# Kernel tuning notes

Measured on AMD Instinct MI355X. Metric: run time of the kernel, lower is better.

The kernel has to match this reference:

```python
import jax, jax.numpy as jnp
import numpy as np

ANCHOR_SIZES = (128.0, 256.0, 512.0)
ASPECT_RATIOS = (0.5, 1.0, 2.0)
NMS_THR = 0.7
KEEP_PRE = 1000    # test_keep_pre_nms
KEEP_POST = 300    # test_keep_post_nms


def make_anchors(fh, fw, img_h, img_w):
    # base anchors per (ratio, size), centered at origin, xyxy
    sizes = jnp.array(ANCHOR_SIZES, jnp.float32)
    ratios = jnp.array(ASPECT_RATIOS, jnp.float32)
    h_r = jnp.sqrt(ratios)
    w_r = 1.0 / h_r
    ws = (w_r[:, None] * sizes[None, :]).reshape(-1)  # [nA]
    hs = (h_r[:, None] * sizes[None, :]).reshape(-1)
    base = jnp.stack([-ws, -hs, ws, hs], axis=1) / 2.0  # [nA,4]
    stride_h = img_h / fh
    stride_w = img_w / fw
    sx = jnp.arange(fw, dtype=jnp.float32) * stride_w
    sy = jnp.arange(fh, dtype=jnp.float32) * stride_h
    yy, xx = jnp.meshgrid(sy, sx, indexing='ij')
    shifts = jnp.stack([xx, yy, xx, yy], axis=-1).reshape(-1, 1, 4)  # [fh*fw,1,4]
    return (shifts + base[None]).reshape(-1, 4)  # [fh*fw*nA,4]


def offsets2boxes(deltas, anchors):
    # deltas: [bs,N,4] (dx,dy,dw,dh); anchors: [N,4] xyxy
    aw = anchors[:, 2] - anchors[:, 0]
    ah = anchors[:, 3] - anchors[:, 1]
    acx = anchors[:, 0] + 0.5 * aw
    acy = anchors[:, 1] + 0.5 * ah
    pcx = deltas[..., 0] * aw + acx
    pcy = deltas[..., 1] * ah + acy
    pw = jnp.exp(deltas[..., 2]) * aw
    ph = jnp.exp(deltas[..., 3]) * ah
    return jnp.stack([pcx - 0.5 * pw, pcy - 0.5 * ph,
                      pcx + 0.5 * pw, pcy + 0.5 * ph], axis=-1)


def nms_single(boxes, scores):
    # boxes [K,4] already sorted by descending score; sequential greedy NMS
    K = boxes.shape[0]
    b = jax.lax.stop_gradient(boxes)
    area = (b[:, 2] - b[:, 0]) * (b[:, 3] - b[:, 1])
    lt = jnp.maximum(b[:, None, :2], b[None, :, :2])
    rb = jnp.minimum(b[:, None, 2:], b[None, :, 2:])
    wh = jnp.clip(rb - lt, 0.0)
    inter = wh[..., 0] * wh[..., 1]
    iou = inter / (area[:, None] + area[None, :] - inter + 1e-9)  # [K,K]
    idx = jnp.arange(K)

    def body(i, keep):
        suppress = (iou[i] > NMS_THR) & keep[i] & (idx > i)
        return keep & ~suppress

    keep = jax.lax.fori_loop(0, K, body, jnp.ones((K,), bool))
    # stable: kept boxes first, preserving score order; pad to KEEP_POST
    order = jnp.argsort((~keep).astype(jnp.int32))[:KEEP_POST]
    valid = keep[order].astype(boxes.dtype)
    dets = jnp.concatenate([boxes[order], scores[order, None]], axis=-1)
    return dets * valid[:, None]  # padded rows are zeros


def setup_inputs() -> dict:
    key = jax.random.key(0)
    ks = jax.random.split(key, 4)
    C = 512
    nA = 9
    return {
        'fmaps': jax.random.normal(ks[0], (8, C, 64, 64), jnp.float32),
        'base_w': jax.random.normal(ks[1], (C, C, 3, 3), jnp.float32) * 0.01,
        'base_b': jnp.zeros((C,), jnp.float32),
        'cls_w': jax.random.normal(ks[2], (nA, C), jnp.float32) * 0.01,
        'cls_b': jnp.zeros((nA,), jnp.float32),
        'reg_w': jax.random.normal(ks[3], (nA * 4, C), jnp.float32) * 0.01,
        'reg_b': jnp.zeros((nA * 4,), jnp.float32),
        'img_h': 1024,
        'img_w': 1024,
    }


def reference(fmaps, base_w, base_b, cls_w, cls_b, reg_w, reg_b, img_h, img_w):
    bs, C, fh, fw = fmaps.shape
    nA = len(ANCHOR_SIZES) * len(ASPECT_RATIOS)
    # PredictionLayer: 3x3 conv + relu, then 1x1 cls / reg convs
    x = jax.lax.conv_general_dilated(
        fmaps, base_w, window_strides=(1, 1), padding='SAME',
        dimension_numbers=('NCHW', 'OIHW', 'NCHW'))
    x = jax.nn.relu(x + base_b[None, :, None, None])
    cls = jnp.einsum('bchw,ac->bahw', x, cls_w) + cls_b[None, :, None, None]
    reg = jnp.einsum('bchw,ac->bahw', x, reg_w) + reg_b[None, :, None, None]
    # flatten_preds: view(bs,nA,c,h,w) -> permute(0,3,4,1,2) -> (bs, h*w*nA, c)
    cls_logits = cls.reshape(bs, nA, 1, fh, fw).transpose(0, 3, 4, 1, 2).reshape(bs, -1, 1)
    reg_deltas = reg.reshape(bs, nA, 4, fh, fw).transpose(0, 3, 4, 1, 2).reshape(bs, -1, 4)
    # DetectionLayer
    anchors = make_anchors(fh, fw, float(img_h), float(img_w))
    scores = jax.nn.sigmoid(cls_logits[..., 0])          # [bs, N]
    boxes = offsets2boxes(reg_deltas, anchors)           # [bs, N, 4]
    _, sel = jax.lax.top_k(scores, KEEP_PRE)             # per-image top-k
    s = jnp.take_along_axis(scores, sel, axis=1)
    b = jnp.take_along_axis(boxes, sel[..., None], axis=1)
    # clip boxes to image
    b = jnp.stack([jnp.clip(b[..., 0], 0.0, float(img_w)),
                   jnp.clip(b[..., 1], 0.0, float(img_h)),
                   jnp.clip(b[..., 2], 0.0, float(img_w)),
                   jnp.clip(b[..., 3], 0.0, float(img_h))], axis=-1)
    # per-image NMS; output padded to fixed [bs, KEEP_POST, 5]
    return jax.vmap(nms_single)(b, s)
```

## Files before the change

### kernel.cpp

```cpp
#include <hip/hip_runtime.h>
#include <math.h>


typedef double f64x4 __attribute__((ext_vector_type(4)));
typedef double f64x2 __attribute__((ext_vector_type(2)));

#define BS 8
#define CIN 512
#define COUT 512
#define FH 64
#define FW 64
#define NA 9
#define NPIX (FH*FW)
#define NANCH (NPIX*NA)
#define NPAD 65536
#define KPRE 1000
#define KPOST 300

#define OFF_X      0ull
#define OFF_SCORES (OFF_X + 134217728ull)
#define OFF_BOXES  (OFF_SCORES + 2359296ull)
#define OFF_KEYS   (OFF_BOXES + 9437184ull)
#define OFF_BUF1   (OFF_KEYS + 4194304ull)
#define OFF_BUF2   (OFF_BUF1 + 1048576ull)
#define OFF_SEL    (OFF_BUF2 + 262144ull)
#define OFF_KEEP   (OFF_SEL + 32768ull)
#define WS_NEEDED  (OFF_KEEP + 32768ull)
#define OFF_MASK   OFF_X
#define WOFF_U        WS_NEEDED
#define WOFF_V        (WOFF_U + 33554432ull)
#define WS_WINO_FULL  (WOFF_V + 67108864ull + 67108864ull)
#define WS_WINO_HALF  (WOFF_V + 33554432ull + 33554432ull)

#define SW_STRIDE 80
#define SW_WORDS  (36 * SW_STRIDE)
#define SI_RSTRIDE 80
#define SI_CSTRIDE 320
#define BUF_WORDS (SW_WORDS + 4 * SI_CSTRIDE)

__device__ __forceinline__ void conv_compute(
    const float* __restrict__ sWp, const float* __restrict__ sIp,
    const int* __restrict__ boff, f64x4 acc[2][4]) {
#pragma unroll
  for (int k0s = 0; k0s < 9; ++k0s) {
    double a0 = (double)sWp[k0s * 4 * SW_STRIDE];
    double a1 = (double)sWp[k0s * 4 * SW_STRIDE + 16];
    const float* bp = sIp + boff[k0s];
    double b0 = (double)bp[0];
    double b1 = (double)bp[16];
    double b2 = (double)bp[32];
    double b3 = (double)bp[48];
    acc[0][0] = __builtin_amdgcn_mfma_f64_16x16x4f64(a0, b0, acc[0][0], 0, 0, 0);
    acc[0][1] = __builtin_amdgcn_mfma_f64_16x16x4f64(a0, b1, acc[0][1], 0, 0, 0);
    acc[0][2] = __builtin_amdgcn_mfma_f64_16x16x4f64(a0, b2, acc[0][2], 0, 0, 0);
    acc[0][3] = __builtin_amdgcn_mfma_f64_16x16x4f64(a0, b3, acc[0][3], 0, 0, 0);
    acc[1][0] = __builtin_amdgcn_mfma_f64_16x16x4f64(a1, b0, acc[1][0], 0, 0, 0);
    acc[1][1] = __builtin_amdgcn_mfma_f64_16x16x4f64(a1, b1, acc[1][1], 0, 0, 0);
    acc[1][2] = __builtin_amdgcn_mfma_f64_16x16x4f64(a1, b2, acc[1][2], 0, 0, 0);
    acc[1][3] = __builtin_amdgcn_mfma_f64_16x16x4f64(a1, b3, acc[1][3], 0, 0, 0);
  }
}

__global__ __launch_bounds__(256, 3) void conv_mfma_kernel(
    const float* __restrict__ fm, const float* __restrict__ W,
    const float* __restrict__ bias, double* __restrict__ x) {
  __shared__ float sbuf[2 * BUF_WORDS];
  const int ocb = blockIdx.x, rp = blockIdx.y, b = blockIdx.z;
  const int h0 = rp * 2;
  const int oc0 = ocb * 64;
  const int tid = threadIdx.x;
  const int wid = tid >> 6, l = tid & 63;
  const int q = l >> 4, r16 = l & 15;
  const int wm = wid >> 1, wn = wid & 1;

  const int wo = tid >> 2, wseg = tid & 3;
  const float* wbase = W + (size_t)(oc0 + wo) * 4608 + wseg * 9;
  const int wlds0 = (wseg * 9) * SW_STRIDE + wo;

  const float* fmb = fm + (size_t)b * CIN * NPIX;
  int ioff[5];
  int idls[5];
  bool sact[5], lact[5];
#pragma unroll
  for (int s = 0; s < 5; ++s) {
    int li = tid + 256 * s;
    sact[s] = li < 1056;
    int li_c = sact[s] ? li : 0;
    int c = li_c / 264, rem = li_c % 264, r = rem / 66, col = rem % 66;
    int gy = h0 - 1 + r, gx = col - 1;
    lact[s] = sact[s] && gy >= 0 && gy < FH && gx >= 0 && gx < FW;
    ioff[s] = lact[s] ? (c * NPIX + gy * FW + gx) : 0;
    idls[s] = SW_WORDS + c * SI_CSTRIDE + r * SI_RSTRIDE + col;
  }

  const int apos = q * SW_STRIDE + wm * 32 + r16;
  const int ipos = SW_WORDS + wn * SI_RSTRIDE + r16;
  int boff[9];
#pragma unroll
  for (int k0s = 0; k0s < 9; ++k0s) {
    int k = k0s * 4 + q;
    int c = k / 9, t = k - 9 * c;
    int dy = t / 3, dx = t - 3 * dy;
    boff[k0s] = c * SI_CSTRIDE + dy * SI_RSTRIDE + dx;
  }

  f64x4 acc[2][4];
#pragma unroll
  for (int tm = 0; tm < 2; ++tm)
#pragma unroll
    for (int tn = 0; tn < 4; ++tn)
#pragma unroll
      for (int v = 0; v < 4; ++v) acc[tm][tn][v] = 0.0;

  float wreg[9], ireg[5];

#define LOAD_REGS(t) do {                                            \
    const int cc_ = 4 * (t);                                         \
    _Pragma("unroll")                                                \
    for (int j = 0; j < 9; ++j) wreg[j] = wbase[cc_ * 9 + j];        \
    _Pragma("unroll")                                                \
    for (int s = 0; s < 5; ++s)                                      \
      ireg[s] = lact[s] ? fmb[(size_t)(ioff[s] + cc_ * NPIX)] : 0.f; \
  } while (0)

#define WRITE_LDS(base) do {                                         \
    _Pragma("unroll")                                                \
    for (int j = 0; j < 9; ++j) (base)[wlds0 + j * SW_STRIDE] = wreg[j]; \
    _Pragma("unroll")                                                \
    for (int s = 0; s < 5; ++s)                                      \
      if (sact[s]) (base)[idls[s]] = ireg[s];                        \
  } while (0)

  float* buf0 = sbuf;
  float* buf1 = sbuf + BUF_WORDS;

  LOAD_REGS(0);
  WRITE_LDS(buf0);
  __syncthreads();

  for (int tt = 0; tt < 64; ++tt) {
    const int t1 = 2 * tt + 1;
    LOAD_REGS(t1);
    __builtin_amdgcn_s_setprio(1);
    conv_compute(buf0 + apos, buf0 + ipos, boff, acc);
    __builtin_amdgcn_s_setprio(0);
    WRITE_LDS(buf1);
    __syncthreads();
    const int t2 = (t1 + 1 < 128) ? t1 + 1 : 127;
    LOAD_REGS(t2);
    __builtin_amdgcn_s_setprio(1);
    conv_compute(buf1 + apos, buf1 + ipos, boff, acc);
    __builtin_amdgcn_s_setprio(0);
    WRITE_LDS(buf0);
    __syncthreads();
  }

  int prow[4], pcol[4];
  {
    f64x4 probe = {0.0, 0.0, 0.0, 0.0};
    double pa = (q == 0) ? (double)r16 : ((q == 1) ? 1.0 : 0.0);
    double pb = (q == 0) ? 1.0 : ((q == 1) ? (double)(16 * r16) : 0.0);
    probe = __builtin_amdgcn_mfma_f64_16x16x4f64(pa, pb, probe, 0, 0, 0);
#pragma unroll
    for (int v = 0; v < 4; ++v) {
      int val = (int)(probe[v] + 0.5);
      prow[v] = val & 15;
      pcol[v] = (val >> 4) & 15;
    }
  }

#pragma unroll
  for (int tm = 0; tm < 2; ++tm) {
#pragma unroll
    for (int v = 0; v < 4; ++v) {
      const int oc = oc0 + wm * 32 + tm * 16 + prow[v];
      const double bv = (double)bias[oc];
      const int h = h0 + wn;
#pragma unroll
      for (int tn = 0; tn < 4; ++tn) {
        const int w = tn * 16 + pcol[v];
        double val = acc[tm][tn][v] + bv;
        val = val > 0.0 ? val : 0.0;
        x[(size_t)(b * COUT + oc) * NPIX + h * FW + w] = val;
      }
    }
  }
#undef LOAD_REGS
#undef WRITE_LDS
}

__global__ __launch_bounds__(256) void wino_wt_kernel(
    const float* __restrict__ W, double* __restrict__ U) {
  const int id = blockIdx.x * 256 + threadIdx.x;
  const int oc = id >> 9, c = id & 511;
  const float* g = W + (size_t)(oc * CIN + c) * 9;
  double g0[3], g1[3], g2[3];
#pragma unroll
  for (int j = 0; j < 3; ++j) {
    g0[j] = (double)g[j];
    g1[j] = (double)g[3 + j];
    g2[j] = (double)g[6 + j];
  }
  double T[4][3];
#pragma unroll
  for (int j = 0; j < 3; ++j) {
    T[0][j] = g0[j];
    T[1][j] = 0.5 * (g0[j] + g1[j] + g2[j]);
    T[2][j] = 0.5 * (g0[j] - g1[j] + g2[j]);
    T[3][j] = g2[j];
  }
  double* Ub = U + (size_t)c * 512 + oc;
#pragma unroll
  for (int xi = 0; xi < 4; ++xi) {
    double u0 = T[xi][0];
    double u1 = 0.5 * (T[xi][0] + T[xi][1] + T[xi][2]);
    double u2 = 0.5 * (T[xi][0] - T[xi][1] + T[xi][2]);
    double u3 = T[xi][2];
    Ub[(size_t)(xi * 4 + 0) * 262144] = u0;
    Ub[(size_t)(xi * 4 + 1) * 262144] = u1;
    Ub[(size_t)(xi * 4 + 2) * 262144] = u2;
    Ub[(size_t)(xi * 4 + 3) * 262144] = u3;
  }
}

template <int T>
__global__ __launch_bounds__(256) void wino_in_kernel(
    const float* __restrict__ fm, double* __restrict__ V, int b, int t0) {
  const int id = blockIdx.x * 256 + threadIdx.x;
  const int c = id / T, rem = id % T;
  const int tyx = t0 + rem;
  const int ty = tyx >> 5, tx = tyx & 31;
  const float* src = fm + (size_t)(b * CIN + c) * NPIX;
  const int y0 = 2 * ty - 1, x0 = 2 * tx - 1;
  double d[4][4];
#pragma unroll
  for (int r = 0; r < 4; ++r) {
    int y = y0 + r;
#pragma unroll
    for (int s = 0; s < 4; ++s) {
      int xx = x0 + s;
      d[r][s] = (y >= 0 && y < FH && xx >= 0 && xx < FW)
                    ? (double)src[y * FW + xx] : 0.0;
    }
  }
  double Z[4][4];
#pragma unroll
  for (int s = 0; s < 4; ++s) {
    Z[0][s] = d[0][s] - d[2][s];
    Z[1][s] = d[1][s] + d[2][s];
    Z[2][s] = d[2][s] - d[1][s];
    Z[3][s] = d[1][s] - d[3][s];
  }
  double* Vb = V + (size_t)c * T + rem;
#pragma unroll
  for (int xi = 0; xi < 4; ++xi) {
    double v0 = Z[xi][0] - Z[xi][2];
    double v1 = Z[xi][1] + Z[xi][2];
    double v2 = Z[xi][2] - Z[xi][1];
    double v3 = Z[xi][1] - Z[xi][3];
    Vb[(size_t)(xi * 4 + 0) * 512 * T] = v0;
    Vb[(size_t)(xi * 4 + 1) * 512 * T] = v1;
    Vb[(size_t)(xi * 4 + 2) * 512 * T] = v2;
    Vb[(size_t)(xi * 4 + 3) * 512 * T] = v3;
  }
}

#define WSU_STRIDE 72
#define WSV_STRIDE 136
#define WSU_WORDS  (8 * WSU_STRIDE)
#define WBUF_WORDS (WSU_WORDS + 8 * WSV_STRIDE)

__device__ __forceinline__ void wino_compute(
    const double* __restrict__ sA, const double* __restrict__ sB,
    f64x4 acc[2][4]) {
#pragma unroll
  for (int kg = 0; kg < 2; ++kg) {
    double a0 = sA[kg * 4 * WSU_STRIDE];
    double a1 = sA[kg * 4 * WSU_STRIDE + 16];
    const double* bp = sB + kg * 4 * WSV_STRIDE;
    double b0 = bp[0];
    double b1 = bp[16];
    double b2 = bp[32];
    double b3 = bp[48];
    acc[0][0] = __builtin_amdgcn_mfma_f64_16x16x4f64(a0, b0, acc[0][0], 0, 0, 0);
    acc[0][1] = __builtin_amdgcn_mfma_f64_16x16x4f64(a0, b1, acc[0][1], 0, 0, 0);
    acc[0][2] = __builtin_amdgcn_mfma_f64_16x16x4f64(a0, b2, acc[0][2], 0, 0, 0);
    acc[0][3] = __builtin_amdgcn_mfma_f64_16x16x4f64(a0, b3, acc[0][3], 0, 0, 0);
    acc[1][0] = __builtin_amdgcn_mfma_f64_16x16x4f64(a1, b0, acc[1][0], 0, 0, 0);
    acc[1][1] = __builtin_amdgcn_mfma_f64_16x16x4f64(a1, b1, acc[1][1], 0, 0, 0);
    acc[1][2] = __builtin_amdgcn_mfma_f64_16x16x4f64(a1, b2, acc[1][2], 0, 0, 0);
    acc[1][3] = __builtin_amdgcn_mfma_f64_16x16x4f64(a1, b3, acc[1][3], 0, 0, 0);
  }
}

template <int T>
__global__ __launch_bounds__(256, 3) void wino_gemm_kernel(
    const double* __restrict__ U, const double* __restrict__ V,
    double* __restrict__ M) {
  __shared__ double sbuf[2 * WBUF_WORDS];
  const int ocb = blockIdx.x, tb = blockIdx.y, pos = blockIdx.z;
  const int oc0 = ocb * 64, t0 = tb * 128;
  const int tid = threadIdx.x;
  const int wid = tid >> 6, l = tid & 63;
  const int q = l >> 4, r16 = l & 15;
  const int wm = wid >> 1, wn = wid & 1;

  const int ka = tid >> 5;
  const int oc2 = (tid & 31) * 2;
  const int t4 = (tid & 31) * 4;
  const double* uSrc = U + (size_t)pos * 262144 + (size_t)ka * 512 + oc0 + oc2;
  const double* vSrc = V + (size_t)pos * 512 * T + (size_t)ka * T + t0 + t4;
  const int ua_lds = ka * WSU_STRIDE + oc2;
  const int vb_lds = WSU_WORDS + ka * WSV_STRIDE + t4;

  const int apos = q * WSU_STRIDE + wm * 32 + r16;
  const int bpos = WSU_WORDS + q * WSV_STRIDE + wn * 64 + r16;

  f64x4 acc[2][4];
#pragma unroll
  for (int tm = 0; tm < 2; ++tm)
#pragma unroll
    for (int tn = 0; tn < 4; ++tn)
#pragma unroll
      for (int v = 0; v < 4; ++v) acc[tm][tn][v] = 0.0;

  f64x2 ra, rb0, rb1;

#define WLOAD(t) do {                                                  \
    const size_t cc_ = 8 * (size_t)(t);                                \
    ra  = *(const f64x2*)(uSrc + cc_ * 512);                           \
    rb0 = *(const f64x2*)(vSrc + cc_ * T);                             \
    rb1 = *(const f64x2*)(vSrc + cc_ * T + 2);                         \
  } while (0)

#define WSTORE(base) do {                                              \
    (base)[ua_lds] = ra[0]; (base)[ua_lds + 1] = ra[1];                \
    (base)[vb_lds] = rb0[0]; (base)[vb_lds + 1] = rb0[1];              \
    (base)[vb_lds + 2] = rb1[0]; (base)[vb_lds + 3] = rb1[1];          \
  } while (0)

  double* buf0 = sbuf;
  double* buf1 = sbuf + WBUF_WORDS;

  WLOAD(0);
  WSTORE(buf0);
  __syncthreads();

  for (int tt = 0; tt < 32; ++tt) {
    const int t1 = 2 * tt + 1;
    WLOAD(t1);
    __builtin_amdgcn_s_setprio(1);
    wino_compute(buf0 + apos, buf0 + bpos, acc);
    __builtin_amdgcn_s_setprio(0);
    WSTORE(buf1);
    __syncthreads();
    const int t2 = (t1 + 1 < 64) ? t1 + 1 : 63;
    WLOAD(t2);
    __builtin_amdgcn_s_setprio(1);
    wino_compute(buf1 + apos, buf1 + bpos, acc);
    __builtin_amdgcn_s_setprio(0);
    WSTORE(buf0);
    __syncthreads();
  }

  int prow[4], pcol[4];
  {
    f64x4 probe = {0.0, 0.0, 0.0, 0.0};
    double pa = (q == 0) ? (double)r16 : ((q == 1) ? 1.0 : 0.0);
    double pb = (q == 0) ? 1.0 : ((q == 1) ? (double)(16 * r16) : 0.0);
    probe = __builtin_amdgcn_mfma_f64_16x16x4f64(pa, pb, probe, 0, 0, 0);
#pragma unroll
    for (int v = 0; v < 4; ++v) {
      int val = (int)(probe[v] + 0.5);
      prow[v] = val & 15;
      pcol[v] = (val >> 4) & 15;
    }
  }

#pragma unroll
  for (int tm = 0; tm < 2; ++tm) {
#pragma unroll
    for (int v = 0; v < 4; ++v) {
      const int oc = oc0 + wm * 32 + tm * 16 + prow[v];
#pragma unroll
      for (int tn = 0; tn < 4; ++tn) {
        const int col = wn * 64 + tn * 16 + pcol[v];
        M[(size_t)pos * 512 * T + (size_t)oc * T + t0 + col] = acc[tm][tn][v];
      }
    }
  }
#undef WLOAD
#undef WSTORE
}

template <int T>
__global__ __launch_bounds__(256) void wino_out_kernel(
    const double* __restrict__ M, const float* __restrict__ bias,
    double* __restrict__ x, int b, int t0) {
  const int id = blockIdx.x * 256 + threadIdx.x;
  const int oc = id / T, rem = id % T;
  const int tyx = t0 + rem;
  const int ty = tyx >> 5, tx = tyx & 31;
  double m[4][4];
#pragma unroll
  for (int xi = 0; xi < 4; ++xi)
#pragma unroll
    for (int nu = 0; nu < 4; ++nu)
      m[xi][nu] = M[(size_t)(xi * 4 + nu) * 512 * T + (size_t)oc * T + rem];
  double P[2][4];
#pragma unroll
  for (int nu = 0; nu < 4; ++nu) {
    P[0][nu] = m[0][nu] + m[1][nu] + m[2][nu];
    P[1][nu] = m[1][nu] - m[2][nu] - m[3][nu];
  }
  const double bv = (double)bias[oc];
  double* xb = x + (size_t)(b * COUT + oc) * NPIX + (2 * ty) * FW + 2 * tx;
#pragma unroll
  for (int i = 0; i < 2; ++i) {
    double y0 = P[i][0] + P[i][1] + P[i][2] + bv;
    double y1 = P[i][1] - P[i][2] - P[i][3] + bv;
    y0 = y0 > 0.0 ? y0 : 0.0;
    y1 = y1 > 0.0 ? y1 : 0.0;
    xb[i * FW] = y0;
    xb[i * FW + 1] = y1;
  }
}

#define HX_STRIDE 72
#define HW_STRIDE 52
#define HSX_WORDS (16 * HX_STRIDE)
#define HBUF_WORDS (HSX_WORDS + 16 * HW_STRIDE)

__device__ __forceinline__ void heads_compute(
    const double* __restrict__ sA, const double* __restrict__ sB,
    f64x4 acc[3]) {
#pragma unroll
  for (int k0s = 0; k0s < 4; ++k0s) {
    double a0 = sA[k0s * 4 * HW_STRIDE];
    double a1 = sA[k0s * 4 * HW_STRIDE + 16];
    double a2 = sA[k0s * 4 * HW_STRIDE + 32];
    double b0 = sB[k0s * 4 * HX_STRIDE];
    acc[0] = __builtin_amdgcn_mfma_f64_16x16x4f64(a0, b0, acc[0], 0, 0, 0);
    acc[1] = __builtin_amdgcn_mfma_f64_16x16x4f64(a1, b0, acc[1], 0, 0, 0);
    acc[2] = __builtin_amdgcn_mfma_f64_16x16x4f64(a2, b0, acc[2], 0, 0, 0);
  }
}

__global__ __launch_bounds__(256) void heads_mfma_kernel(
    const double* __restrict__ x, const float* __restrict__ cls_w,
    const float* __restrict__ cls_b, const float* __restrict__ reg_w,
    const float* __restrict__ reg_b, const int* __restrict__ img_h,
    const int* __restrict__ img_w, double* __restrict__ scores,
    double* __restrict__ boxes, unsigned long long* __restrict__ keys) {
  __shared__ double sh[2 * HBUF_WORDS];
  const int pxb = blockIdx.x, b = blockIdx.y;
  const int tid = threadIdx.x;
  const int wid = tid >> 6, l = tid & 63;
  const int q = l >> 4, r16 = l & 15;
  const int wn = wid;

  const double* xbase = x + (size_t)b * CIN * NPIX + pxb * 64;
  int sxk[4], sxp[4];
#pragma unroll
  for (int s = 0; s < 4; ++s) {
    int i = tid + 256 * s;
    sxk[s] = i >> 6; sxp[s] = i & 63;
  }
  int swk[3], swo[3];
#pragma unroll
  for (int s = 0; s < 3; ++s) {
    int i = tid + 256 * s;
    swk[s] = i / 48; swo[s] = i % 48;
  }

  const int aposh = HSX_WORDS + q * HW_STRIDE + r16;
  const int bposh = q * HX_STRIDE + wn * 16 + r16;

  f64x4 acc[3];
#pragma unroll
  for (int mt = 0; mt < 3; ++mt)
#pragma unroll
    for (int v = 0; v < 4; ++v) acc[mt][v] = 0.0;

  double xr[4], wr[3];

#define HLOAD(t) do {                                                    \
    const int cc_ = 16 * (t);                                            \
    _Pragma("unroll")                                                    \
    for (int s = 0; s < 4; ++s)                                          \
      xr[s] = xbase[(size_t)(cc_ + sxk[s]) * NPIX + sxp[s]];             \
    _Pragma("unroll")                                                    \
    for (int s = 0; s < 3; ++s) {                                        \
      int o = swo[s], k = cc_ + swk[s];                                  \
      wr[s] = (o < 9) ? (double)cls_w[o * CIN + k]                       \
            : (o < 45) ? (double)reg_w[(o - 9) * CIN + k] : 0.0;         \
    }                                                                    \
  } while (0)

#define HSTORE(base) do {                                                \
    _Pragma("unroll")                                                    \
    for (int s = 0; s < 4; ++s) (base)[sxk[s] * HX_STRIDE + sxp[s]] = xr[s]; \
    _Pragma("unroll")                                                    \
    for (int s = 0; s < 3; ++s)                                          \
      (base)[HSX_WORDS + swk[s] * HW_STRIDE + swo[s]] = wr[s];           \
  } while (0)

  double* buf0 = sh;
  double* buf1 = sh + HBUF_WORDS;

  HLOAD(0);
  HSTORE(buf0);
  __syncthreads();

  for (int tt = 0; tt < 16; ++tt) {
    const int t1 = 2 * tt + 1;
    HLOAD(t1);
    __builtin_amdgcn_s_setprio(1);
    heads_compute(buf0 + aposh, buf0 + bposh, acc);
    __builtin_amdgcn_s_setprio(0);
    HSTORE(buf1);
    __syncthreads();
    const int t2 = (t1 + 1 < 32) ? t1 + 1 : 31;
    HLOAD(t2);
    __builtin_amdgcn_s_setprio(1);
    heads_compute(buf1 + aposh, buf1 + bposh, acc);
    __builtin_amdgcn_s_setprio(0);
    HSTORE(buf0);
    __syncthreads();
  }

  int prow[4], pcol[4];
  {
    f64x4 probe = {0.0, 0.0, 0.0, 0.0};
    double pa = (q == 0) ? (double)r16 : ((q == 1) ? 1.0 : 0.0);
    double pb = (q == 0) ? 1.0 : ((q == 1) ? (double)(16 * r16) : 0.0);
    probe = __builtin_amdgcn_mfma_f64_16x16x4f64(pa, pb, probe, 0, 0, 0);
#pragma unroll
    for (int v = 0; v < 4; ++v) {
      int val = (int)(probe[v] + 0.5);
      prow[v] = val & 15;
      pcol[v] = (val >> 4) & 15;
    }
  }

  double* slog = sh;
#pragma unroll
  for (int mt = 0; mt < 3; ++mt) {
#pragma unroll
    for (int v = 0; v < 4; ++v) {
      const int o = mt * 16 + prow[v];
      if (o < 45) {
        double bv = (o < 9) ? (double)cls_b[o] : (double)reg_b[o - 9];
        slog[o * HX_STRIDE + wn * 16 + pcol[v]] = acc[mt][v] + bv;
      }
    }
  }
  __syncthreads();

  const double ih = (double)img_h[0], iw = (double)img_w[0];
  const double sth = ih / (double)FH, stw = iw / (double)FW;
  const double ratios[3] = {0.5, 1.0, 2.0};
  const double sizes[3] = {128.0, 256.0, 512.0};

  for (int it = tid; it < 576; it += 256) {
    int px = it / 9, a = it % 9;
    int p = pxb * 64 + px;
    int hh = p >> 6, ww = p & 63;
    double z = slog[a * HX_STRIDE + px];
    double score = 1.0 / (1.0 + exp(-z));
    double d0 = slog[(9 + a * 4 + 0) * HX_STRIDE + px];
    double d1 = slog[(9 + a * 4 + 1) * HX_STRIDE + px];
    double d2 = slog[(9 + a * 4 + 2) * HX_STRIDE + px];
    double d3 = slog[(9 + a * 4 + 3) * HX_STRIDE + px];
    double ratio = ratios[a / 3], size = sizes[a % 3];
    double hr = sqrt(ratio), wr_ = 1.0 / hr;
    double wsz = wr_ * size, hsz = hr * size;
    double sxc = (double)ww * stw, syc = (double)hh * sth;
    double ax0 = sxc - wsz * 0.5, ax1 = sxc + wsz * 0.5;
    double ay0 = syc - hsz * 0.5, ay1 = syc + hsz * 0.5;
    double aw = ax1 - ax0, ah = ay1 - ay0;
    double acx = ax0 + 0.5 * aw, acy = ay0 + 0.5 * ah;
    double pcx = d0 * aw + acx, pcy = d1 * ah + acy;
    double pw = exp(d2) * aw, ph = exp(d3) * ah;
    double bx0 = pcx - 0.5 * pw, by0 = pcy - 0.5 * ph;
    double bx1 = pcx + 0.5 * pw, by1 = pcy + 0.5 * ph;
    bx0 = fmin(fmax(bx0, 0.0), iw); bx1 = fmin(fmax(bx1, 0.0), iw);
    by0 = fmin(fmax(by0, 0.0), ih); by1 = fmin(fmax(by1, 0.0), ih);
    long n = (long)p * 9 + a;
    long base = (long)b * NANCH + n;
    boxes[base * 4 + 0] = bx0; boxes[base * 4 + 1] = by0;
    boxes[base * 4 + 2] = bx1; boxes[base * 4 + 3] = by1;
    scores[base] = score;
    unsigned long long bits = (unsigned long long)__double_as_longlong(score);
    keys[(long)b * NPAD + n] =
        ~((bits & 0xFFFFFFFFFFFF0000ull) | (0xFFFFull - (unsigned long long)n));
  }
#undef HLOAD
#undef HSTORE
}

__device__ inline void bitonic4096(unsigned long long* s, int tid) {
  for (int k = 2; k <= 4096; k <<= 1) {
    for (int j = k >> 1; j > 0; j >>= 1) {
#pragma unroll 2
      for (int t = tid; t < 2048; t += 1024) {
        int i = ((t & ~(j - 1)) << 1) | (t & (j - 1));
        int p = i | j;
        bool up = ((i & k) == 0);
        unsigned long long a = s[i], c = s[p];
        if ((a > c) == up) { s[i] = c; s[p] = a; }
      }
      __syncthreads();
    }
  }
}

__global__ __launch_bounds__(1024) void sort_topk_kernel(
    const unsigned long long* __restrict__ in, unsigned long long* __restrict__ out,
    long in_stride, long out_stride) {
  __shared__ unsigned long long s[4096];
  const int b = blockIdx.y, q = blockIdx.x, tid = threadIdx.x;
  const unsigned long long* ip = in + (long)b * in_stride + (long)q * 4096;
#pragma unroll 4
  for (int l = tid; l < 4096; l += 1024) s[l] = ip[l];
  __syncthreads();
  bitonic4096(s, tid);
  unsigned long long* op = out + (long)b * out_stride + (long)q * 1024;
  op[tid] = s[tid];
}

__global__ __launch_bounds__(1024) void sort_final_kernel(
    const unsigned long long* __restrict__ in, int* __restrict__ sel) {
  __shared__ unsigned long long s[4096];
  const int b = blockIdx.x, tid = threadIdx.x;
  const unsigned long long* ip = in + (long)b * 4096;
#pragma unroll 4
  for (int l = tid; l < 4096; l += 1024) s[l] = ip[l];
  __syncthreads();
  bitonic4096(s, tid);
  if (tid < KPRE) sel[b * 1024 + tid] = (int)(s[tid] & 0xFFFFull);
}

__global__ __launch_bounds__(256) void nms_mask_kernel(
    const double* __restrict__ boxes, const int* __restrict__ sel,
    unsigned long long* __restrict__ mask) {
  __shared__ double X0[KPRE], Y0[KPRE], X1[KPRE], Y1[KPRE], AR[KPRE];
  const int ig = blockIdx.x, b = blockIdx.y, tid = threadIdx.x;
  for (int r = tid; r < KPRE; r += 256) {
    int n = sel[b * 1024 + r];
    const double* bp = boxes + ((long)b * NANCH + n) * 4;
    double x0 = bp[0], y0 = bp[1], x1 = bp[2], y1 = bp[3];
    X0[r] = x0; Y0[r] = y0; X1[r] = x1; Y1[r] = y1;
    AR[r] = (x1 - x0) * (y1 - y0);
  }
  __syncthreads();
  const int i = ig * 16 + (tid >> 4);
  const int w = tid & 15;
  if (i >= KPRE) return;
  const double xi0 = X0[i], yi0 = Y0[i], xi1 = X1[i], yi1 = Y1[i], ai = AR[i];
  unsigned long long m = 0;
#pragma unroll 8
  for (int jj = 0; jj < 64; ++jj) {
    int jo = (jj + w) & 63;
    int j = w * 64 + jo;
    if (j < KPRE && j > i) {
      double lx = fmax(xi0, X0[j]), ly = fmax(yi0, Y0[j]);
      double rx = fmin(xi1, X1[j]), ry = fmin(yi1, Y1[j]);
      double ww_ = fmax(rx - lx, 0.0);
      double hh_ = fmax(ry - ly, 0.0);
      double inter = ww_ * hh_;
      double iou = inter / (ai + AR[j] - inter + 1e-9);
      if (iou > 0.7) m |= (1ull << jo);
    }
  }
  mask[((size_t)b * 1024 + i) * 16 + w] = m;
}

__global__ __launch_bounds__(256) void nms_scan_kernel(
    const unsigned long long* __restrict__ mask, int* __restrict__ keep) {
  __shared__ unsigned long long smask[16384];
  __shared__ unsigned long long skeep[16];
  const int b = blockIdx.x, tid = threadIdx.x;
  const unsigned long long* mb = mask + (size_t)b * 1024 * 16;
  for (int l = tid; l < KPRE * 16; l += 256) smask[l] = mb[l];
  __syncthreads();
  if (tid < 64) {
    const int lane16 = tid & 15;
    unsigned long long mykeep = ~0ull;
    unsigned long long p0, p1, p2, p3, p4, p5, p6, p7,
                       p8, p9, p10, p11, p12, p13, p14, p15;
    p0  = smask[0 * 16 + lane16];  p1  = smask[1 * 16 + lane16];
    p2  = smask[2 * 16 + lane16];  p3  = smask[3 * 16 + lane16];
    p4  = smask[4 * 16 + lane16];  p5  = smask[5 * 16 + lane16];
    p6  = smask[6 * 16 + lane16];  p7  = smask[7 * 16 + lane16];
    p8  = smask[8 * 16 + lane16];  p9  = smask[9 * 16 + lane16];
    p10 = smask[10 * 16 + lane16]; p11 = smask[11 * 16 + lane16];
    p12 = smask[12 * 16 + lane16]; p13 = smask[13 * 16 + lane16];
    p14 = smask[14 * 16 + lane16]; p15 = smask[15 * 16 + lane16];
#define NMS_STEP(j) do {                                                   \
      const int ii = i + (j);                                              \
      unsigned long long kw = __shfl(mykeep, ii >> 6);                     \
      bool on = (ii < KPRE) && ((kw >> (ii & 63)) & 1ull);                 \
      mykeep &= ~(on ? p##j : 0ull);                                       \
      p##j = smask[(ii + 16) * 16 + lane16];                               \
    } while (0)
    for (int i = 0; i < 1008; i += 16) {
      NMS_STEP(0);  NMS_STEP(1);  NMS_STEP(2);  NMS_STEP(3);
      NMS_STEP(4);  NMS_STEP(5);  NMS_STEP(6);  NMS_STEP(7);
      NMS_STEP(8);  NMS_STEP(9);  NMS_STEP(10); NMS_STEP(11);
      NMS_STEP(12); NMS_STEP(13); NMS_STEP(14); NMS_STEP(15);
    }
#undef NMS_STEP
    if (tid < 16) skeep[tid] = mykeep;
  }
  __syncthreads();
  for (int r = tid; r < KPRE; r += 256)
    keep[b * 1024 + r] = (int)((skeep[r >> 6] >> (r & 63)) & 1ull);
}

__global__ __launch_bounds__(1024) void out_kernel(
    const double* __restrict__ boxes, const double* __restrict__ scores,
    const int* __restrict__ sel, const int* __restrict__ keep,
    float* __restrict__ out) {
  const int b = blockIdx.x, tid = threadIdx.x;
  int kv = (tid < KPRE) ? keep[b * 1024 + tid] : 0;
  unsigned long long m = __ballot(kv != 0);
  int lane = tid & 63, wid = tid >> 6;
  __shared__ int wcnt[16], woff[16], tot;
  if (lane == 0) wcnt[wid] = __popcll(m);
  __syncthreads();
  if (tid == 0) {
    int s = 0;
    for (int w2 = 0; w2 < 16; ++w2) { woff[w2] = s; s += wcnt[w2]; }
    tot = s;
  }
  __syncthreads();
  int before = __popcll(m & ((1ull << lane) - 1ull));
  int pref = woff[wid] + before;
  if (tid < KPRE) {
    int pos = kv ? pref : (tot + (tid - pref));
    if (pos < KPOST) {
      float* o = out + ((long)b * KPOST + pos) * 5;
      if (kv) {
        int n = sel[b * 1024 + tid];
        const double* bp = boxes + ((long)b * NANCH + n) * 4;
        o[0] = (float)bp[0]; o[1] = (float)bp[1];
        o[2] = (float)bp[2]; o[3] = (float)bp[3];
        o[4] = (float)scores[(long)b * NANCH + n];
      } else {
        o[0] = 0.f; o[1] = 0.f; o[2] = 0.f; o[3] = 0.f; o[4] = 0.f;
      }
    }
  }
}

extern "C" void kernel_launch(void* const* d_in, const int* in_sizes, int n_in,
                              void* d_out, int out_size, void* d_ws, size_t ws_size,
                              hipStream_t stream) {
  const float* fm     = (const float*)d_in[0];
  const float* base_w = (const float*)d_in[1];
  const float* base_b = (const float*)d_in[2];
  const float* cls_w  = (const float*)d_in[3];
  const float* cls_b  = (const float*)d_in[4];
  const float* reg_w  = (const float*)d_in[5];
  const float* reg_b  = (const float*)d_in[6];
  const int* img_h    = (const int*)d_in[7];
  const int* img_w    = (const int*)d_in[8];
  float* out          = (float*)d_out;

  if (ws_size < WS_NEEDED) return;

  char* ws = (char*)d_ws;
  double* x                 = (double*)(ws + OFF_X);
  double* scores            = (double*)(ws + OFF_SCORES);
  double* boxes             = (double*)(ws + OFF_BOXES);
  unsigned long long* keys  = (unsigned long long*)(ws + OFF_KEYS);
  unsigned long long* buf1  = (unsigned long long*)(ws + OFF_BUF1);
  unsigned long long* buf2  = (unsigned long long*)(ws + OFF_BUF2);
  int* sel                  = (int*)(ws + OFF_SEL);
  int* keep                 = (int*)(ws + OFF_KEEP);
  unsigned long long* mask  = (unsigned long long*)(ws + OFF_MASK);

  hipMemsetAsync(ws + OFF_KEYS, 0xFF, 4194304ull + 1048576ull, stream);

  if (ws_size >= WS_WINO_FULL) {
    double* U = (double*)(ws + WOFF_U);
    double* V = (double*)(ws + WOFF_V);
    double* M = (double*)(ws + WOFF_V + 67108864ull);
    wino_wt_kernel<<<dim3(1024), dim3(256), 0, stream>>>(base_w, U);
    for (int b = 0; b < BS; ++b) {
      wino_in_kernel<1024><<<dim3(2048), dim3(256), 0, stream>>>(fm, V, b, 0);
      wino_gemm_kernel<1024><<<dim3(8, 8, 16), dim3(256), 0, stream>>>(U, V, M);
      wino_out_kernel<1024><<<dim3(2048), dim3(256), 0, stream>>>(M, base_b, x, b, 0);
    }
  } else if (ws_size >= WS_WINO_HALF) {
    double* U = (double*)(ws + WOFF_U);
    double* V = (double*)(ws + WOFF_V);
    double* M = (double*)(ws + WOFF_V + 33554432ull);
    wino_wt_kernel<<<dim3(1024), dim3(256), 0, stream>>>(base_w, U);
    for (int b = 0; b < BS; ++b) {
      for (int t0 = 0; t0 < 1024; t0 += 512) {
        wino_in_kernel<512><<<dim3(1024), dim3(256), 0, stream>>>(fm, V, b, t0);
        wino_gemm_kernel<512><<<dim3(8, 4, 16), dim3(256), 0, stream>>>(U, V, M);
        wino_out_kernel<512><<<dim3(1024), dim3(256), 0, stream>>>(M, base_b, x, b, t0);
      }
    }
  } else {
    conv_mfma_kernel<<<dim3(8, 32, 8), dim3(256), 0, stream>>>(fm, base_w, base_b, x);
  }

  heads_mfma_kernel<<<dim3(64, 8), dim3(256), 0, stream>>>(
      x, cls_w, cls_b, reg_w, reg_b, img_h, img_w, scores, boxes, keys);
  sort_topk_kernel<<<dim3(9, 8), dim3(1024), 0, stream>>>(keys, buf1, 65536, 16384);
  sort_topk_kernel<<<dim3(4, 8), dim3(1024), 0, stream>>>(buf1, buf2, 16384, 4096);
  sort_final_kernel<<<dim3(8), dim3(1024), 0, stream>>>(buf2, sel);
  nms_mask_kernel<<<dim3(64, 8), dim3(256), 0, stream>>>(boxes, sel, mask);
  nms_scan_kernel<<<dim3(8), dim3(256), 0, stream>>>(mask, keep);
  out_kernel<<<dim3(8), dim3(1024), 0, stream>>>(boxes, scores, sel, keep, out);
}
```

Baseline: 1.740 ms.

## Fuse Winograd input transform into the batched GEMM kernel

Removes the separate Winograd input-transform kernel and its double-precision V buffer. The GEMM kernel now loads raw float feature-map rows into shared memory and computes each transformed element on the fly from four neighbours with sign FMAs. This cuts the global write and reread of V, but each of the 16 Winograd positions reloads the input tile and redoes the transform. The half-workspace Winograd path is dropped, so smaller workspaces fall back to the direct convolution.

```diff
diff --git a/kernel.cpp b/kernel.cpp
--- a/kernel.cpp
+++ b/kernel.cpp
@@ -27,10 +27,9 @@
 #define OFF_KEEP   (OFF_SEL + 32768ull)
 #define WS_NEEDED  (OFF_KEEP + 32768ull)
 #define OFF_MASK   OFF_X
-#define WOFF_U        WS_NEEDED
-#define WOFF_V        (WOFF_U + 33554432ull)
-#define WS_WINO_FULL  (WOFF_V + 67108864ull + 67108864ull)
-#define WS_WINO_HALF  (WOFF_V + 33554432ull + 33554432ull)
+#define WOFF_U     WS_NEEDED
+#define WOFF_M     (WOFF_U + 33554432ull)
+#define WS_FUSED   (WOFF_M + 67108864ull)
 
 #define SW_STRIDE 80
 #define SW_WORDS  (36 * SW_STRIDE)
@@ -223,98 +222,53 @@
   }
 }
 
-template <int T>
-__global__ __launch_bounds__(256) void wino_in_kernel(
-    const float* __restrict__ fm, double* __restrict__ V, int b, int t0) {
-  const int id = blockIdx.x * 256 + threadIdx.x;
-  const int c = id / T, rem = id % T;
-  const int tyx = t0 + rem;
-  const int ty = tyx >> 5, tx = tyx & 31;
-  const float* src = fm + (size_t)(b * CIN + c) * NPIX;
-  const int y0 = 2 * ty - 1, x0 = 2 * tx - 1;
-  double d[4][4];
-#pragma unroll
-  for (int r = 0; r < 4; ++r) {
-    int y = y0 + r;
-#pragma unroll
-    for (int s = 0; s < 4; ++s) {
-      int xx = x0 + s;
-      d[r][s] = (y >= 0 && y < FH && xx >= 0 && xx < FW)
-                    ? (double)src[y * FW + xx] : 0.0;
-    }
-  }
-  double Z[4][4];
-#pragma unroll
-  for (int s = 0; s < 4; ++s) {
-    Z[0][s] = d[0][s] - d[2][s];
-    Z[1][s] = d[1][s] + d[2][s];
-    Z[2][s] = d[2][s] - d[1][s];
-    Z[3][s] = d[1][s] - d[3][s];
-  }
-  double* Vb = V + (size_t)c * T + rem;
-#pragma unroll
-  for (int xi = 0; xi < 4; ++xi) {
-    double v0 = Z[xi][0] - Z[xi][2];
-    double v1 = Z[xi][1] + Z[xi][2];
-    double v2 = Z[xi][2] - Z[xi][1];
-    double v3 = Z[xi][1] - Z[xi][3];
-    Vb[(size_t)(xi * 4 + 0) * 512 * T] = v0;
-    Vb[(size_t)(xi * 4 + 1) * 512 * T] = v1;
-    Vb[(size_t)(xi * 4 + 2) * 512 * T] = v2;
-    Vb[(size_t)(xi * 4 + 3) * 512 * T] = v3;
-  }
-}
-
-#define WSU_STRIDE 72
-#define WSV_STRIDE 136
-#define WSU_WORDS  (8 * WSU_STRIDE)
-#define WBUF_WORDS (WSU_WORDS + 8 * WSV_STRIDE)
-
-__device__ __forceinline__ void wino_compute(
-    const double* __restrict__ sA, const double* __restrict__ sB,
-    f64x4 acc[2][4]) {
-#pragma unroll
-  for (int kg = 0; kg < 2; ++kg) {
-    double a0 = sA[kg * 4 * WSU_STRIDE];
-    double a1 = sA[kg * 4 * WSU_STRIDE + 16];
-    const double* bp = sB + kg * 4 * WSV_STRIDE;
-    double b0 = bp[0];
-    double b1 = bp[16];
-    double b2 = bp[32];
-    double b3 = bp[48];
-    acc[0][0] = __builtin_amdgcn_mfma_f64_16x16x4f64(a0, b0, acc[0][0], 0, 0, 0);
-    acc[0][1] = __builtin_amdgcn_mfma_f64_16x16x4f64(a0, b1, acc[0][1], 0, 0, 0);
-    acc[0][2] = __builtin_amdgcn_mfma_f64_16x16x4f64(a0, b2, acc[0][2], 0, 0, 0);
-    acc[0][3] = __builtin_amdgcn_mfma_f64_16x16x4f64(a0, b3, acc[0][3], 0, 0, 0);
-    acc[1][0] = __builtin_amdgcn_mfma_f64_16x16x4f64(a1, b0, acc[1][0], 0, 0, 0);
-    acc[1][1] = __builtin_amdgcn_mfma_f64_16x16x4f64(a1, b1, acc[1][1], 0, 0, 0);
-    acc[1][2] = __builtin_amdgcn_mfma_f64_16x16x4f64(a1, b2, acc[1][2], 0, 0, 0);
-    acc[1][3] = __builtin_amdgcn_mfma_f64_16x16x4f64(a1, b3, acc[1][3], 0, 0, 0);
-  }
-}
-
-template <int T>
-__global__ __launch_bounds__(256, 3) void wino_gemm_kernel(
-    const double* __restrict__ U, const double* __restrict__ V,
-    double* __restrict__ M) {
-  __shared__ double sbuf[2 * WBUF_WORDS];
-  const int ocb = blockIdx.x, tb = blockIdx.y, pos = blockIdx.z;
-  const int oc0 = ocb * 64, t0 = tb * 128;
+__global__ __launch_bounds__(256, 3) void wino_fgemm_kernel(
+    const float* __restrict__ fm, const double* __restrict__ U,
+    double* __restrict__ M, int b) {
+  __shared__ __attribute__((aligned(16))) double sU2[2][576];
+  __shared__ __attribute__((aligned(16))) float  sF2[2][5440];
+  const int tb = blockIdx.x, ocb = blockIdx.y, pos = blockIdx.z;
+  const int oc0 = ocb * 64;
   const int tid = threadIdx.x;
   const int wid = tid >> 6, l = tid & 63;
   const int q = l >> 4, r16 = l & 15;
   const int wm = wid >> 1, wn = wid & 1;
-
-  const int ka = tid >> 5;
-  const int oc2 = (tid & 31) * 2;
-  const int t4 = (tid & 31) * 4;
-  const double* uSrc = U + (size_t)pos * 262144 + (size_t)ka * 512 + oc0 + oc2;
-  const double* vSrc = V + (size_t)pos * 512 * T + (size_t)ka * T + t0 + t4;
-  const int ua_lds = ka * WSU_STRIDE + oc2;
-  const int vb_lds = WSU_WORDS + ka * WSV_STRIDE + t4;
-
-  const int apos = q * WSU_STRIDE + wm * 32 + r16;
-  const int bpos = WSU_WORDS + q * WSV_STRIDE + wn * 64 + r16;
+  const int xi = pos >> 2, nu = pos & 3;
+
+  const int rAt[4] = {0, 1, 2, 1}, rBt[4] = {2, 2, 1, 3};
+  const double sTt[4] = {-1.0, 1.0, -1.0, -1.0};
+  const int rA68 = rAt[xi] * 68, rB68 = rBt[xi] * 68;
+  const int cA = rAt[nu], cB = rBt[nu];
+  const double sgnR = sTt[xi], sgnC = sTt[nu];
+
+  int bofft[4];
+#pragma unroll
+  for (int tn = 0; tn < 4; ++tn) {
+    int tyl = wn * 2 + (tn >> 1);
+    int tx = (tn & 1) * 16 + r16;
+    bofft[tn] = tyl * 136 + tx * 2 + 1;
+  }
+  const int qb = q * 680;
+
+  const int apos = q * 72 + wm * 32 + r16;
+
+  int goff[10], ldso[10];
+  bool lok[10];
+#pragma unroll
+  for (int s = 0; s < 10; ++s) {
+    int row = (tid >> 5) + 8 * s;
+    int seg = tid & 31;
+    int c = row / 10, pr = row % 10;
+    int y = 8 * tb - 1 + pr;
+    lok[s] = (y >= 0 && y < FH);
+    goff[s] = c * NPIX + y * FW + seg * 2;
+    ldso[s] = c * 680 + pr * 68 + 2 + seg * 2;
+  }
+  const float* fmb = fm + (size_t)b * CIN * NPIX;
+  const double* ub = U + (size_t)pos * 262144 + oc0 + (tid >> 5) * 512 + (tid & 31) * 2;
+  const int uoff = (tid >> 5) * 72 + (tid & 31) * 2;
+
+  for (int i = tid; i < 5440; i += 256) { sF2[0][i] = 0.f; sF2[1][i] = 0.f; }
 
   f64x4 acc[2][4];
 #pragma unroll
@@ -324,42 +278,71 @@
 #pragma unroll
       for (int v = 0; v < 4; ++v) acc[tm][tn][v] = 0.0;
 
-  f64x2 ra, rb0, rb1;
-
-#define WLOAD(t) do {                                                  \
-    const size_t cc_ = 8 * (size_t)(t);                                \
-    ra  = *(const f64x2*)(uSrc + cc_ * 512);                           \
-    rb0 = *(const f64x2*)(vSrc + cc_ * T);                             \
-    rb1 = *(const f64x2*)(vSrc + cc_ * T + 2);                         \
+  float2 fr[10];
+  f64x2 ur;
+
+#define FLOAD(t) do {                                                      \
+    const int cc_ = 8 * (t);                                               \
+    _Pragma("unroll")                                                      \
+    for (int s = 0; s < 10; ++s)                                           \
+      fr[s] = lok[s] ? *(const float2*)(fmb + (size_t)cc_ * NPIX + goff[s])\
+                     : make_float2(0.f, 0.f);                              \
+    ur = *(const f64x2*)(ub + (size_t)cc_ * 512);                          \
   } while (0)
 
-#define WSTORE(base) do {                                              \
-    (base)[ua_lds] = ra[0]; (base)[ua_lds + 1] = ra[1];                \
-    (base)[vb_lds] = rb0[0]; (base)[vb_lds + 1] = rb0[1];              \
-    (base)[vb_lds + 2] = rb1[0]; (base)[vb_lds + 3] = rb1[1];          \
+#define FSTORE(pF, pU) do {                                                \
+    _Pragma("unroll")                                                      \
+    for (int s = 0; s < 10; ++s) *(float2*)((pF) + ldso[s]) = fr[s];       \
+    *(f64x2*)((pU) + uoff) = ur;                                           \
   } while (0)
 
-  double* buf0 = sbuf;
-  double* buf1 = sbuf + WBUF_WORDS;
-
-  WLOAD(0);
-  WSTORE(buf0);
+#define FCOMPUTE(pF, pU) do {                                              \
+    _Pragma("unroll")                                                      \
+    for (int kg = 0; kg < 2; ++kg) {                                       \
+      double a0 = (pU)[apos + kg * 288];                                   \
+      double a1 = (pU)[apos + kg * 288 + 16];                              \
+      double bf[4];                                                        \
+      _Pragma("unroll")                                                    \
+      for (int tn = 0; tn < 4; ++tn) {                                     \
+        const float* p = (pF) + kg * 2720 + qb + bofft[tn];                \
+        double d1 = (double)p[rA68 + cA];                                  \
+        double d2 = (double)p[rB68 + cA];                                  \
+        double d3 = (double)p[rA68 + cB];                                  \
+        double d4 = (double)p[rB68 + cB];                                  \
+        double t1 = fma(sgnR, d2, d1);                                     \
+        double t2 = fma(sgnR, d4, d3);                                     \
+        bf[tn] = fma(sgnC, t2, t1);                                        \
+      }                                                                    \
+      acc[0][0] = __builtin_amdgcn_mfma_f64_16x16x4f64(a0, bf[0], acc[0][0], 0, 0, 0); \
+      acc[0][1] = __builtin_amdgcn_mfma_f64_16x16x4f64(a0, bf[1], acc[0][1], 0, 0, 0); \
+      acc[0][2] = __builtin_amdgcn_mfma_f64_16x16x4f64(a0, bf[2], acc[0][2], 0, 0, 0); \
+      acc[0][3] = __builtin_amdgcn_mfma_f64_16x16x4f64(a0, bf[3], acc[0][3], 0, 0, 0); \
+      acc[1][0] = __builtin_amdgcn_mfma_f64_16x16x4f64(a1, bf[0], acc[1][0], 0, 0, 0); \
+      acc[1][1] = __builtin_amdgcn_mfma_f64_16x16x4f64(a1, bf[1], acc[1][1], 0, 0, 0); \
+      acc[1][2] = __builtin_amdgcn_mfma_f64_16x16x4f64(a1, bf[2], acc[1][2], 0, 0, 0); \
+      acc[1][3] = __builtin_amdgcn_mfma_f64_16x16x4f64(a1, bf[3], acc[1][3], 0, 0, 0); \
+    }                                                                      \
+  } while (0)
+
+  FLOAD(0);
+  __syncthreads();
+  FSTORE(sF2[0], sU2[0]);
   __syncthreads();
 
   for (int tt = 0; tt < 32; ++tt) {
     const int t1 = 2 * tt + 1;
-    WLOAD(t1);
+    FLOAD(t1);
     __builtin_amdgcn_s_setprio(1);
-    wino_compute(buf0 + apos, buf0 + bpos, acc);
+    FCOMPUTE(sF2[0], sU2[0]);
     __builtin_amdgcn_s_setprio(0);
-    WSTORE(buf1);
+    FSTORE(sF2[1], sU2[1]);
     __syncthreads();
     const int t2 = (t1 + 1 < 64) ? t1 + 1 : 63;
-    WLOAD(t2);
+    FLOAD(t2);
     __builtin_amdgcn_s_setprio(1);
-    wino_compute(buf1 + apos, buf1 + bpos, acc);
+    FCOMPUTE(sF2[1], sU2[1]);
     __builtin_amdgcn_s_setprio(0);
-    WSTORE(buf0);
+    FSTORE(sF2[0], sU2[0]);
     __syncthreads();
   }
 
@@ -384,13 +367,14 @@
       const int oc = oc0 + wm * 32 + tm * 16 + prow[v];
 #pragma unroll
       for (int tn = 0; tn < 4; ++tn) {
-        const int col = wn * 64 + tn * 16 + pcol[v];
-        M[(size_t)pos * 512 * T + (size_t)oc * T + t0 + col] = acc[tm][tn][v];
+        const int col = tb * 128 + wn * 64 + tn * 16 + pcol[v];
+        M[(size_t)pos * 524288 + (size_t)oc * 1024 + col] = acc[tm][tn][v];
       }
     }
   }
-#undef WLOAD
-#undef WSTORE
+#undef FLOAD
+#undef FSTORE
+#undef FCOMPUTE
 }
 
 template <int T>
@@ -783,27 +767,13 @@
 
   hipMemsetAsync(ws + OFF_KEYS, 0xFF, 4194304ull + 1048576ull, stream);
 
-  if (ws_size >= WS_WINO_FULL) {
+  if (ws_size >= WS_FUSED) {
     double* U = (double*)(ws + WOFF_U);
-    double* V = (double*)(ws + WOFF_V);
-    double* M = (double*)(ws + WOFF_V + 67108864ull);
+    double* M = (double*)(ws + WOFF_M);
     wino_wt_kernel<<<dim3(1024), dim3(256), 0, stream>>>(base_w, U);
     for (int b = 0; b < BS; ++b) {
-      wino_in_kernel<1024><<<dim3(2048), dim3(256), 0, stream>>>(fm, V, b, 0);
-      wino_gemm_kernel<1024><<<dim3(8, 8, 16), dim3(256), 0, stream>>>(U, V, M);
+      wino_fgemm_kernel<<<dim3(8, 8, 16), dim3(256), 0, stream>>>(fm, U, M, b);
       wino_out_kernel<1024><<<dim3(2048), dim3(256), 0, stream>>>(M, base_b, x, b, 0);
-    }
-  } else if (ws_size >= WS_WINO_HALF) {
-    double* U = (double*)(ws + WOFF_U);
-    double* V = (double*)(ws + WOFF_V);
-    double* M = (double*)(ws + WOFF_V + 33554432ull);
-    wino_wt_kernel<<<dim3(1024), dim3(256), 0, stream>>>(base_w, U);
-    for (int b = 0; b < BS; ++b) {
-      for (int t0 = 0; t0 < 1024; t0 += 512) {
-        wino_in_kernel<512><<<dim3(1024), dim3(256), 0, stream>>>(fm, V, b, t0);
-        wino_gemm_kernel<512><<<dim3(8, 4, 16), dim3(256), 0, stream>>>(U, V, M);
-        wino_out_kernel<512><<<dim3(1024), dim3(256), 0, stream>>>(M, base_b, x, b, t0);
-      }
     }
   } else {
     conv_mfma_kernel<<<dim3(8, 32, 8), dim3(256), 0, stream>>>(fm, base_w, base_b, x);
```

Result: slower. 2.995 ms (+72.2%).
